# Optimization experiments

Measured on AMD Instinct MI355X. Metric: run time of the kernel, lower is better.

## Reference

```python
import jax, jax.numpy as jnp
import numpy as np

IN_DIM = 512
RATIO = 8
QK_DIM = IN_DIM // RATIO  # 64
B, C, H, W = 8, IN_DIM, 64, 64


def setup_inputs() -> dict:
    key = jax.random.key(0)
    ks = jax.random.split(key, 9)
    x = jax.random.normal(ks[0], (B, C, H, W), dtype=jnp.float32)
    y = jax.random.normal(ks[1], (B, C, H, W), dtype=jnp.float32)
    z = jax.random.normal(ks[2], (B, C, H, W), dtype=jnp.float32)
    # 1x1 conv weights, xavier_normal with gain=0.02: std = gain*sqrt(2/(fan_in+fan_out))
    def xavier(k, out_c, in_c, gain=0.02):
        std = gain * np.sqrt(2.0 / (in_c + out_c))
        return jax.random.normal(k, (out_c, in_c), dtype=jnp.float32) * std
    Wq = xavier(ks[3], QK_DIM, C)
    Wk = xavier(ks[4], QK_DIM, C)
    Wv = xavier(ks[5], C, C)
    bq = jnp.zeros((QK_DIM,), dtype=jnp.float32)
    bk = jnp.zeros((QK_DIM,), dtype=jnp.float32)
    bv = jnp.zeros((C,), dtype=jnp.float32)
    gamma = jnp.zeros((1,), dtype=jnp.float32)
    return {"x": x, "y": y, "z": z, "Wq": Wq, "bq": bq, "Wk": Wk,
            "bk": bk, "Wv": Wv, "bv": bv, "gamma": gamma}


def reference(x, y, z, Wq, bq, Wk, bk, Wv, bv, gamma):
    b, c, h, w = x.shape
    n = h * w
    # 1x1 convs == per-pixel linear projections
    q = (jnp.einsum('oc,bchw->bohw', Wq, x) + bq[None, :, None, None]).reshape(b, -1, n)  # [B, d, N]
    k = (jnp.einsum('oc,bchw->bohw', Wk, y) + bk[None, :, None, None]).reshape(b, -1, n)  # [B, d, N]
    v = (jnp.einsum('oc,bchw->bohw', Wv, z) + bv[None, :, None, None]).reshape(b, -1, n)  # [B, C, N]
    # energy[b, i, j] = <q[:, i], k[:, j]>, no scaling (matches original)
    energy = jnp.einsum('bdn,bdm->bnm', q, k)      # [B, N, N]
    attention = jax.nn.softmax(energy, axis=-1)     # softmax over keys
    # out = value @ attention^T : out[:, c, i] = sum_j v[:, c, j] * attention[:, i, j]
    out = jnp.einsum('bcj,bij->bci', v, attention)  # [B, C, N]
    out = out.reshape(b, c, h, w)
    out = gamma[0] * out + x
    return out
```

## Files before the change

### kernel.cpp

```cpp
#include <hip/hip_runtime.h>
#include <hip/hip_bf16.h>
#include <hip/hip_fp8.h>
#include <stdint.h>

#define B_   8
#define C_   512
#define NPIX 4096
#define VLDB 4160

typedef __attribute__((ext_vector_type(8))) short bf16x8;
typedef __attribute__((ext_vector_type(4))) float f32x4;

__device__ __forceinline__ uint16_t f2bf(float f) {
    union { float f; uint32_t u; } v; v.f = f;
    uint32_t u = v.u;
    return (uint16_t)((u + 0x7FFFu + ((u >> 16) & 1u)) >> 16);
}

__device__ __forceinline__ uint32_t pk2(float a, float b) {
    union { __hip_bfloat162 h; uint32_t u; } c;
    c.h = __float22bfloat162_rn(make_float2(a, b));
    return c.u;
}

__device__ __forceinline__ float fexp2(float x) {
#if __has_builtin(__builtin_amdgcn_exp2f)
    return __builtin_amdgcn_exp2f(x);
#else
    return exp2f(x);
#endif
}

template<bool HI>
__device__ __forceinline__ uint32_t pk_fp8(float a, float b, uint32_t old) {
#if __has_builtin(__builtin_amdgcn_cvt_pk_fp8_f32)
    return __builtin_amdgcn_cvt_pk_fp8_f32(a, b, old, HI);
#else
    union { __hip_fp8_storage_t s[4]; uint32_t u; } r; r.u = old;
    r.s[HI * 2 + 0] = __hip_cvt_float_to_fp8(a, __HIP_SATFINITE, __HIP_E4M3);
    r.s[HI * 2 + 1] = __hip_cvt_float_to_fp8(b, __HIP_SATFINITE, __HIP_E4M3);
    return r.u;
#endif
}
__device__ __forceinline__ uint8_t f2fp8(float a) {
#if __has_builtin(__builtin_amdgcn_cvt_pk_fp8_f32)
    uint32_t u = __builtin_amdgcn_cvt_pk_fp8_f32(a, 0.f, 0u, false);
    return (uint8_t)(u & 0xFF);
#else
    return __hip_cvt_float_to_fp8(a, __HIP_SATFINITE, __HIP_E4M3);
#endif
}

template<bool TRANS>
__global__ __launch_bounds__(256, 2) void proj_kernel(
    const float* __restrict__ X, const float* __restrict__ W,
    const float* __restrict__ bias, uint8_t* __restrict__ outp,
    int O, float scale)
{
    __shared__ char xt[64 * 128];
    const int b  = blockIdx.z;
    const int o0 = blockIdx.y * 64;
    const int n0 = blockIdx.x * 64;
    const int t = threadIdx.x, w = t >> 6, l = t & 63;
    const int l15 = l & 15, lg = l >> 4;
    const float* Xb = X + (size_t)b * C_ * NPIX + n0;

    f32x4 acc[4] = {};

    for (int cc = 0; cc < C_; cc += 64) {
        __syncthreads();
        #pragma unroll
        for (int i = 0; i < 16; i += 2) {
            int c = w * 16 + i;
            float f0 = Xb[(size_t)(cc + c) * NPIX + l];
            float f1 = Xb[(size_t)(cc + c + 1) * NPIX + l];
            uint32_t pair = pk2(f0, f1);
            int byte = (l * 128 + c * 2) ^ ((l & 7) << 4);
            *(uint32_t*)(xt + byte) = pair;
        }
        __syncthreads();
        #pragma unroll
        for (int kk = 0; kk < 2; kk++) {
            int o  = o0 + w * 16 + l15;
            int cb = cc + kk * 32 + lg * 8;
            float4 wa = *(const float4*)&W[(size_t)o * C_ + cb];
            float4 wb = *(const float4*)&W[(size_t)o * C_ + cb + 4];
            union { bf16x8 v; uint32_t u[4]; } afu;
            afu.u[0] = pk2(wa.x, wa.y); afu.u[1] = pk2(wa.z, wa.w);
            afu.u[2] = pk2(wb.x, wb.y); afu.u[3] = pk2(wb.z, wb.w);
            #pragma unroll
            for (int jt = 0; jt < 4; jt++) {
                int n = jt * 16 + l15;
                int byte = (n * 128 + (kk * 32 + lg * 8) * 2) ^ ((n & 7) << 4);
                bf16x8 bfr = *(bf16x8*)(xt + byte);
                acc[jt] = __builtin_amdgcn_mfma_f32_16x16x32_bf16(afu.v, bfr, acc[jt], 0, 0, 0);
            }
        }
    }
    int og = o0 + w * 16 + lg * 4;
    #pragma unroll
    for (int jt = 0; jt < 4; jt++) {
        int n = n0 + jt * 16 + l15;
        #pragma unroll
        for (int r = 0; r < 4; r++) {
            float v = (acc[jt][r] + bias[og + r]) * scale;
            if (TRANS) {
                ((uint16_t*)outp)[((size_t)b * NPIX + n) * 64 + og + r] = f2bf(v);
            } else {
                int j6 = n & 63;
                int pos = ((j6 >> 3) & 3) * 16 + ((j6 >> 5) << 3) + (j6 & 7);
                outp[((size_t)b * (size_t)O + og + r) * (size_t)VLDB + (size_t)(n >> 6) * 64 + pos] = f2fp8(v);
            }
        }
    }
}

__global__ __launch_bounds__(256, 2) void attn_kernel(
    const uint16_t* __restrict__ qT, const uint16_t* __restrict__ kT,
    const uint8_t* __restrict__ vB, const float* __restrict__ X,
    const float* __restrict__ gamma_p, float* __restrict__ out)
{
    __shared__ char  Pl[3][64 * 64];
    __shared__ float lsum[64][5];

    const int id  = blockIdx.x;
    const int xcd = id & 7, slot = id >> 3;
    const int g   = xcd + 8 * (slot >> 6);
    const int qt  = slot & 63;
    const int b   = g >> 1, cb = g & 1;
    const int i0  = qt * 64;

    const int t = threadIdx.x, w = t >> 6, l = t & 63;
    const int l15 = l & 15, lg = l >> 4;
    const int c0 = cb * 256 + w * 64;

    auto barrier_lds = [&]() {
        asm volatile("s_waitcnt lgkmcnt(0)" ::: "memory");
        __builtin_amdgcn_s_barrier();
    };

    bf16x8 q8[4][2];
    #pragma unroll
    for (int it = 0; it < 4; it++)
        #pragma unroll
        for (int kk = 0; kk < 2; kk++)
            q8[it][kk] = *(const bf16x8*)&qT[((size_t)b * NPIX + i0 + it*16 + l15) * 64 + kk*32 + lg*8];

    f32x4 oacc[4][4] = {};
    float l_part[4] = {0.f, 0.f, 0.f, 0.f};

    const uint16_t* kTb = kT + (size_t)b * NPIX * 64;
    const uint8_t*  vBb = vB + ((size_t)b * C_ + c0) * (size_t)VLDB + lg * 16;
    const uint16_t* kROW = kTb + (size_t)(w * 16 + l15) * 64 + lg * 8;

    int vrowB[4];
    #pragma unroll
    for (int ct = 0; ct < 4; ct++) vrowB[ct] = (ct * 16 + l15) * VLDB;

    bf16x8 k8[2];
    ulong2 vreg[4];
    f32x4 s[4];

    auto loadK = [&](int step) {
        const uint16_t* p = kROW + (size_t)step * (64 * 64);
        k8[0] = *(const bf16x8*)p;
        k8[1] = *(const bf16x8*)(p + 32);
    };
    auto loadV = [&](int step) {
        const uint8_t* p = vBb + (size_t)step * 64;
        #pragma unroll
        for (int ct = 0; ct < 4; ct++)
            vreg[ct] = *(const ulong2*)(p + vrowB[ct]);
    };
    auto QK = [&]() {
        #pragma unroll
        for (int it = 0; it < 4; it++) s[it] = f32x4{0.f, 0.f, 0.f, 0.f};
        __builtin_amdgcn_s_setprio(1);
        #pragma unroll
        for (int kk = 0; kk < 2; kk++)
            #pragma unroll
            for (int it = 0; it < 4; it++)
                s[it] = __builtin_amdgcn_mfma_f32_16x16x32_bf16(k8[kk], q8[it][kk], s[it], 0, 0, 0);
        __builtin_amdgcn_s_setprio(0);
    };
    auto PcomputeWrite = [&](char* Pn) {
        #pragma unroll
        for (int it = 0; it < 4; it++) {
            float e0 = fexp2(fminf(s[it][0], 60.f));
            float e1 = fexp2(fminf(s[it][1], 60.f));
            float e2 = fexp2(fminf(s[it][2], 60.f));
            float e3 = fexp2(fminf(s[it][3], 60.f));
            l_part[it] += (e0 + e1) + (e2 + e3);
            uint32_t p4 = pk_fp8<false>(e0, e1, 0u);
            p4 = pk_fp8<true>(e2, e3, p4);
            int i = it * 16 + l15;
            int byte = (i * 64 + w * 16 + lg * 4) ^ ((i & 7) << 3);
            *(uint32_t*)(Pn + byte) = p4;
        }
    };
    auto PV = [&](const char* P) {
        __builtin_amdgcn_s_setprio(1);
        #pragma unroll
        for (int kk = 0; kk < 2; kk++) {
            long pb[4];
            #pragma unroll
            for (int it = 0; it < 4; it++) {
                int i = it * 16 + l15;
                int byte = (i * 64 + kk * 32 + lg * 8) ^ ((i & 7) << 3);
                pb[it] = *(const long*)(P + byte);
            }
            #pragma unroll
            for (int ct = 0; ct < 4; ct++) {
                long v8 = (long)(kk ? vreg[ct].y : vreg[ct].x);
                #pragma unroll
                for (int it = 0; it < 4; it++)
                    oacc[ct][it] = __builtin_amdgcn_mfma_f32_16x16x32_fp8_fp8(v8, pb[it], oacc[ct][it], 0, 0, 0);
            }
        }
        __builtin_amdgcn_s_setprio(0);
    };

    loadK(0);
    loadV(0);
    QK();
    loadK(1);
    PcomputeWrite(Pl[0]);
    QK();
    loadK(2);
    PcomputeWrite(Pl[1]);

    char* Pprev = Pl[0];
    char* Pcur  = Pl[1];
    char* Pnext = Pl[2];

    #pragma unroll 1
    for (int jt_ = 1; jt_ < 64; ++jt_) {
        barrier_lds();
        PV(Pprev);
        loadV(jt_);
        if (jt_ < 63) {
            QK();
            if (jt_ < 62) loadK(jt_ + 2);
            PcomputeWrite(Pnext);
        }
        char* tmp = Pprev; Pprev = Pcur; Pcur = Pnext; Pnext = tmp;
    }
    barrier_lds();
    PV(Pprev);

    #pragma unroll
    for (int it = 0; it < 4; it++) {
        float v = l_part[it];
        v += __shfl_xor(v, 16);
        v += __shfl_xor(v, 32);
        if (lg == 0) lsum[it * 16 + l15][w] = v;
    }
    __syncthreads();

    float gamma = gamma_p[0];
    float rl[4];
    #pragma unroll
    for (int it = 0; it < 4; it++) {
        int i = it * 16 + l15;
        rl[it] = 1.0f / (64.0f * ((lsum[i][0] + lsum[i][1]) + (lsum[i][2] + lsum[i][3])));
    }
    #pragma unroll
    for (int ct = 0; ct < 4; ct++)
        #pragma unroll
        for (int r = 0; r < 4; r++) {
            int c = c0 + ct * 16 + lg * 4 + r;
            #pragma unroll
            for (int it = 0; it < 4; it++) {
                int n = i0 + it * 16 + l15;
                size_t idx = ((size_t)b * C_ + c) * NPIX + n;
                out[idx] = gamma * (oacc[ct][it][r] * rl[it]) + X[idx];
            }
        }
}

extern "C" void kernel_launch(void* const* d_in, const int* in_sizes, int n_in,
                              void* d_out, int out_size, void* d_ws, size_t ws_size,
                              hipStream_t stream) {
    const float* x     = (const float*)d_in[0];
    const float* y     = (const float*)d_in[1];
    const float* z     = (const float*)d_in[2];
    const float* Wq    = (const float*)d_in[3];
    const float* bq    = (const float*)d_in[4];
    const float* Wk    = (const float*)d_in[5];
    const float* bk    = (const float*)d_in[6];
    const float* Wv    = (const float*)d_in[7];
    const float* bv    = (const float*)d_in[8];
    const float* gamma = (const float*)d_in[9];
    float* out = (float*)d_out;

    uint16_t* qT = (uint16_t*)d_ws;
    uint16_t* kT = qT + (size_t)B_ * NPIX * 64;
    uint8_t*  vb = (uint8_t*)(kT + (size_t)B_ * NPIX * 64);

    proj_kernel<true ><<<dim3(64, 1, 8), dim3(256), 0, stream>>>(x, Wq, bq, (uint8_t*)qT, 64, 1.4426950408889634f);
    proj_kernel<true ><<<dim3(64, 1, 8), dim3(256), 0, stream>>>(y, Wk, bk, (uint8_t*)kT, 64, 1.0f);
    proj_kernel<false><<<dim3(64, 8, 8), dim3(256), 0, stream>>>(z, Wv, bv, vb, 512, 64.0f);
    attn_kernel<<<dim3(1024), dim3(256), 0, stream>>>(qT, kT, vb, x, gamma, out);
}
```

Measured before the change: 281.6 us.

## Stage full z pixel tile in LDS once and loop over all V output channels

The V projection previously launched 8 output-channel blocks per pixel tile, each re-reading and re-converting the same 64-pixel slice of z from global memory. A dedicated projv kernel now loads the whole 512-channel by 64-pixel bf16 tile into 64 KB of shared memory once, then iterates over all output-channel groups serially. This removes redundant global reads of z, but cuts the grid to 512 blocks, and the larger LDS footprint lowers occupancy and leaves less parallelism to hide latency.

```diff
diff --git a/kernel.cpp b/kernel.cpp
--- a/kernel.cpp
+++ b/kernel.cpp
@@ -51,15 +51,13 @@
 #endif
 }
 
-template<bool TRANS>
 __global__ __launch_bounds__(256, 2) void proj_kernel(
     const float* __restrict__ X, const float* __restrict__ W,
-    const float* __restrict__ bias, uint8_t* __restrict__ outp,
-    int O, float scale)
+    const float* __restrict__ bias, uint16_t* __restrict__ out,
+    float scale)
 {
     __shared__ char xt[64 * 128];
     const int b  = blockIdx.z;
-    const int o0 = blockIdx.y * 64;
     const int n0 = blockIdx.x * 64;
     const int t = threadIdx.x, w = t >> 6, l = t & 63;
     const int l15 = l & 15, lg = l >> 4;
@@ -81,7 +79,7 @@
         __syncthreads();
         #pragma unroll
         for (int kk = 0; kk < 2; kk++) {
-            int o  = o0 + w * 16 + l15;
+            int o  = w * 16 + l15;
             int cb = cc + kk * 32 + lg * 8;
             float4 wa = *(const float4*)&W[(size_t)o * C_ + cb];
             float4 wb = *(const float4*)&W[(size_t)o * C_ + cb + 4];
@@ -97,19 +95,74 @@
             }
         }
     }
-    int og = o0 + w * 16 + lg * 4;
+    int og = w * 16 + lg * 4;
     #pragma unroll
     for (int jt = 0; jt < 4; jt++) {
         int n = n0 + jt * 16 + l15;
         #pragma unroll
         for (int r = 0; r < 4; r++) {
             float v = (acc[jt][r] + bias[og + r]) * scale;
-            if (TRANS) {
-                ((uint16_t*)outp)[((size_t)b * NPIX + n) * 64 + og + r] = f2bf(v);
-            } else {
-                int j6 = n & 63;
-                int pos = ((j6 >> 3) & 3) * 16 + ((j6 >> 5) << 3) + (j6 & 7);
-                outp[((size_t)b * (size_t)O + og + r) * (size_t)VLDB + (size_t)(n >> 6) * 64 + pos] = f2fp8(v);
+            out[((size_t)b * NPIX + n) * 64 + og + r] = f2bf(v);
+        }
+    }
+}
+
+__global__ __launch_bounds__(256, 2) void projv_kernel(
+    const float* __restrict__ X, const float* __restrict__ W,
+    const float* __restrict__ bias, uint8_t* __restrict__ outp)
+{
+    __shared__ char xt[64 * 1024];
+    const int b  = blockIdx.z;
+    const int n0 = blockIdx.x * 64;
+    const int t = threadIdx.x, w = t >> 6, l = t & 63;
+    const int l15 = l & 15, lg = l >> 4;
+    const float* Xb = X + (size_t)b * C_ * NPIX + n0;
+
+    for (int cc = 0; cc < C_; cc += 64) {
+        #pragma unroll
+        for (int i = 0; i < 16; i += 2) {
+            int c = cc + w * 16 + i;
+            float f0 = Xb[(size_t)c * NPIX + l];
+            float f1 = Xb[(size_t)(c + 1) * NPIX + l];
+            uint32_t pair = pk2(f0, f1);
+            int byte = (l * 1024 + c * 2) ^ ((l & 7) << 4);
+            *(uint32_t*)(xt + byte) = pair;
+        }
+    }
+    __syncthreads();
+
+    #pragma unroll 1
+    for (int o0 = 0; o0 < C_; o0 += 64) {
+        f32x4 acc[4] = {};
+        #pragma unroll 1
+        for (int cc = 0; cc < C_; cc += 64) {
+            #pragma unroll
+            for (int kk = 0; kk < 2; kk++) {
+                int o  = o0 + w * 16 + l15;
+                int cb = cc + kk * 32 + lg * 8;
+                float4 wa = *(const float4*)&W[(size_t)o * C_ + cb];
+                float4 wb = *(const float4*)&W[(size_t)o * C_ + cb + 4];
+                union { bf16x8 v; uint32_t u[4]; } afu;
+                afu.u[0] = pk2(wa.x, wa.y); afu.u[1] = pk2(wa.z, wa.w);
+                afu.u[2] = pk2(wb.x, wb.y); afu.u[3] = pk2(wb.z, wb.w);
+                #pragma unroll
+                for (int jt = 0; jt < 4; jt++) {
+                    int n = jt * 16 + l15;
+                    int byte = (n * 1024 + cb * 2) ^ ((n & 7) << 4);
+                    bf16x8 bfr = *(bf16x8*)(xt + byte);
+                    acc[jt] = __builtin_amdgcn_mfma_f32_16x16x32_bf16(afu.v, bfr, acc[jt], 0, 0, 0);
+                }
+            }
+        }
+        int og = o0 + w * 16 + lg * 4;
+        #pragma unroll
+        for (int jt = 0; jt < 4; jt++) {
+            int j6 = jt * 16 + l15;
+            int pos = ((j6 >> 3) & 3) * 16 + ((j6 >> 5) << 3) + (j6 & 7);
+            #pragma unroll
+            for (int r = 0; r < 4; r++) {
+                float v = (acc[jt][r] + bias[og + r]) * 64.0f;
+                outp[((size_t)b * C_ + og + r) * (size_t)VLDB + (size_t)(n0 >> 6) * 64 + pos] = f2fp8(v);
             }
         }
     }
@@ -297,8 +350,8 @@
     uint16_t* kT = qT + (size_t)B_ * NPIX * 64;
     uint8_t*  vb = (uint8_t*)(kT + (size_t)B_ * NPIX * 64);
 
-    proj_kernel<true ><<<dim3(64, 1, 8), dim3(256), 0, stream>>>(x, Wq, bq, (uint8_t*)qT, 64, 1.4426950408889634f);
-    proj_kernel<true ><<<dim3(64, 1, 8), dim3(256), 0, stream>>>(y, Wk, bk, (uint8_t*)kT, 64, 1.0f);
-    proj_kernel<false><<<dim3(64, 8, 8), dim3(256), 0, stream>>>(z, Wv, bv, vb, 512, 64.0f);
-    attn_kernel<<<dim3(1024), dim3(256), 0, stream>>>(qT, kT, vb, x, gamma, out);
-}
+    proj_kernel <<<dim3(64, 1, 8), dim3(256), 0, stream>>>(x, Wq, bq, qT, 1.4426950408889634f);
+    proj_kernel <<<dim3(64, 1, 8), dim3(256), 0, stream>>>(y, Wk, bk, kT, 1.0f);
+    projv_kernel<<<dim3(64, 1, 8), dim3(256), 0, stream>>>(z, Wv, bv, vb);
+    attn_kernel <<<dim3(1024), dim3(256), 0, stream>>>(qT, kT, vb, x, gamma, out);
+}
```

New measurement: 266.0 us. 1.06x faster.
